# Kernel optimization log

Measured on AMD Instinct MI355X. Metric: run time of the kernel, lower is better.

The kernel has to match this reference:

```python
import jax, jax.numpy as jnp
import numpy as np

BS, N, H = 8, 2048, 512
NEG_INF = -1.0e9
LEAKY_SLOPE = 0.01  # torch nn.LeakyReLU default


def setup_inputs() -> dict:
    key = jax.random.key(0)
    ks = jax.random.split(key, 8)
    feats = jax.random.normal(ks[0], (BS, N, H), dtype=jnp.float32)
    # random 0/1 adjacency with self-loops so every row has >=1 neighbor
    adj = jax.random.randint(ks[1], (BS, N, N), 0, 2).astype(jnp.float32)
    adj = jnp.maximum(adj, jnp.eye(N, dtype=jnp.float32)[None])
    s = 1.0 / np.sqrt(H)
    return {
        "feats": feats,
        "adj_mat": adj,
        "fc_w": jax.random.normal(ks[2], (H, H), dtype=jnp.float32) * s,
        "fc_b": jax.random.normal(ks[3], (H,), dtype=jnp.float32) * s,
        "q_w": jax.random.normal(ks[4], (1, H), dtype=jnp.float32) * s,
        "q_b": jax.random.normal(ks[5], (1,), dtype=jnp.float32) * s,
        "k_w": jax.random.normal(ks[6], (1, H), dtype=jnp.float32) * s,
        "k_b": jax.random.normal(ks[7], (1,), dtype=jnp.float32) * s,
    }


def reference(feats, adj_mat, fc_w, fc_b, q_w, q_b, k_w, k_b):
    # feats: [bs, N, H]; torch Linear: x @ W.T + b
    feat_proj = jnp.einsum("bnh,oh->bno", feats, fc_w) + fc_b          # [bs, N, H]
    q = jnp.einsum("bnh,oh->bno", feat_proj, q_w) + q_b                # [bs, N, 1]
    k = jnp.einsum("bnh,oh->bno", feat_proj, k_w) + k_b                # [bs, N, 1]
    logits = q + jnp.swapaxes(k, 2, 1)                                 # [bs, N, N] broadcast add
    masked = logits + (1.0 - adj_mat) * NEG_INF
    masked = jnp.where(masked >= 0, masked, LEAKY_SLOPE * masked)      # LeakyReLU
    atten = jax.nn.softmax(masked, axis=-1)
    # dropout is identity in eval mode
    out = jnp.einsum("bnm,bmh->bnh", atten, feat_proj)
    return out + feats  # residual=True
```

## Files before the change

kernel.cpp:

```cpp
#include <hip/hip_runtime.h>
#include <hip/hip_bf16.h>
#include <cstdint>
#include <cstddef>

#define BSZ 8
#define NN 2048
#define HH 512
#define MROWS (BSZ * NN)
#define LOG2E 1.44269504088896f

typedef __attribute__((ext_vector_type(4))) float f32x4;
typedef __attribute__((ext_vector_type(8))) short short8;
typedef __attribute__((ext_vector_type(4))) unsigned short us4;
typedef __attribute__((ext_vector_type(4))) uint32_t u32x4;

#if __has_builtin(__builtin_amdgcn_exp2f)
#define EXP2(x) __builtin_amdgcn_exp2f(x)
#else
#define EXP2(x) __expf((x) * 0.69314718056f)
#endif

static __device__ __forceinline__ unsigned short f2bf(float f) {
    uint32_t u = __builtin_bit_cast(uint32_t, f);
    u += 0x7fffu + ((u >> 16) & 1u);
    return (unsigned short)(u >> 16);
}

static __device__ __forceinline__ void async16(const unsigned short* g, unsigned short* l) {
    __builtin_amdgcn_global_load_lds(
        (const __attribute__((address_space(1))) void*)g,
        (__attribute__((address_space(3))) void*)l, 16, 0, 0);
}

__global__ __launch_bounds__(256) void prep_kernel(
    const float* __restrict__ feats, const float* __restrict__ fc_w,
    unsigned short* __restrict__ feats_bf, unsigned short* __restrict__ fcw_bf) {
    const int bid = blockIdx.x;
    const int tid = threadIdx.x;
    if (bid < 2048) {
        const int base = bid * 1024 + tid;
#pragma unroll
        for (int j = 0; j < 4; ++j) {
            const int i = base + j * 256;
            f32x4 v = ((const f32x4*)feats)[i];
            us4 o;
#pragma unroll
            for (int c = 0; c < 4; ++c) o[c] = f2bf(v[c]);
            ((us4*)feats_bf)[i] = o;
        }
    } else {
        const int base = (bid - 2048) * 1024 + tid;
#pragma unroll
        for (int j = 0; j < 4; ++j) {
            const int i = base + j * 256;
            f32x4 v = ((const f32x4*)fc_w)[i];
            us4 o;
#pragma unroll
            for (int c = 0; c < 4; ++c) o[c] = f2bf(v[c]);
            ((us4*)fcw_bf)[i] = o;
        }
    }
}

__global__ __launch_bounds__(256) void k2_kernel(
    const unsigned short* __restrict__ A, const unsigned short* __restrict__ Bt,
    const float* __restrict__ fc_b, const float* __restrict__ q_w,
    const float* __restrict__ k_w, const float* __restrict__ adj,
    unsigned short* __restrict__ fpT, unsigned char* __restrict__ maskb,
    float* __restrict__ qpart, float* __restrict__ kpart) {
    __shared__ alignas(16) unsigned short As[3][64 * 32];
    __shared__ alignas(16) unsigned short Bs[3][128 * 32];
    __shared__ float qred[2][64], kred[2][64];
    const int bid = blockIdx.x;
    const int tid = threadIdx.x;
    const int wave = tid >> 6, lane = tid & 63;
    if (bid % 3 == 0) {
        const int g = bid / 3;
        const int wi = wave >> 1, wj = wave & 1;
        const int n0 = (g & 3) * 128;
        const int i0 = (g >> 2) * 64;
        const int K = HH;
        const int lrow = lane >> 2;
        const int lseg = (lane & 3) * 8;
        const int fro = (lane & 15) * 32 + (lane >> 4) * 8;
        f32x4 acc[2][4];
#pragma unroll
        for (int a = 0; a < 2; ++a)
#pragma unroll
            for (int c = 0; c < 4; ++c) acc[a][c] = (f32x4)(0.f);

        auto stage = [&](int buf, int k0) {
            const unsigned short* ga = A + (size_t)(i0 + wave * 16 + lrow) * K + k0 + lseg;
            async16(ga, &As[buf][(wave * 16) * 32]);
            const unsigned short* gb = Bt + (size_t)(n0 + wave * 32 + lrow) * K + k0 + lseg;
            async16(gb, &Bs[buf][(wave * 32) * 32]);
            async16(gb + (size_t)16 * K, &Bs[buf][(wave * 32 + 16) * 32]);
        };

        stage(0, 0);
        asm volatile("s_waitcnt vmcnt(0)" ::: "memory");
        __builtin_amdgcn_sched_barrier(0);
        __builtin_amdgcn_s_barrier();
        __builtin_amdgcn_sched_barrier(0);

        for (int j = 0; j < 16; ++j) {
            if (j < 15) {
                stage((j + 1) % 3, (j + 1) * 32);
                asm volatile("s_waitcnt vmcnt(3)" ::: "memory");
            } else {
                asm volatile("s_waitcnt vmcnt(0)" ::: "memory");
            }
            __builtin_amdgcn_sched_barrier(0);
            __builtin_amdgcn_s_barrier();
            __builtin_amdgcn_sched_barrier(0);
            const int p = j % 3;
            short8 af[2], bf[4];
#pragma unroll
            for (int t = 0; t < 2; ++t) af[t] = *(const short8*)&As[p][(wi * 32 + t * 16) * 32 + fro];
#pragma unroll
            for (int t = 0; t < 4; ++t) bf[t] = *(const short8*)&Bs[p][(wj * 64 + t * 16) * 32 + fro];
            __builtin_amdgcn_s_setprio(1);
#pragma unroll
            for (int it = 0; it < 2; ++it)
#pragma unroll
                for (int jt = 0; jt < 4; ++jt)
                    acc[it][jt] = __builtin_amdgcn_mfma_f32_16x16x32_bf16(af[it], bf[jt], acc[it][jt], 0, 0, 0);
            __builtin_amdgcn_s_setprio(0);
        }

        int colv[4]; float cbv[4], qwv[4], kwv[4];
#pragma unroll
        for (int jt = 0; jt < 4; ++jt) {
            colv[jt] = n0 + wj * 64 + jt * 16 + (lane & 15);
            cbv[jt] = fc_b[colv[jt]];
            qwv[jt] = q_w[colv[jt]];
            kwv[jt] = k_w[colv[jt]];
        }
        const int b = i0 >> 11;
        const int il = i0 & 2047;
#pragma unroll
        for (int jt = 0; jt < 4; ++jt) {
#pragma unroll
            for (int it = 0; it < 2; ++it) {
                const int rb = wi * 32 + it * 16 + ((lane >> 4) << 2);
                us4 o;
#pragma unroll
                for (int r = 0; r < 4; ++r) o[r] = f2bf(acc[it][jt][r] + cbv[jt]);
                *(us4*)(fpT + ((size_t)b * HH + colv[jt]) * NN + il + rb) = o;
            }
        }
#pragma unroll
        for (int it = 0; it < 2; ++it) {
#pragma unroll
            for (int r = 0; r < 4; ++r) {
                float pq = 0.f, pk = 0.f;
#pragma unroll
                for (int jt = 0; jt < 4; ++jt) {
                    float v = acc[it][jt][r] + cbv[jt];
                    pq += v * qwv[jt];
                    pk += v * kwv[jt];
                }
                for (int off = 1; off < 16; off <<= 1) {
                    pq += __shfl_xor(pq, off, 64);
                    pk += __shfl_xor(pk, off, 64);
                }
                if ((lane & 15) == 0) {
                    const int rr = wi * 32 + it * 16 + ((lane >> 4) << 2) + r;
                    qred[wj][rr] = pq;
                    kred[wj][rr] = pk;
                }
            }
        }
        __syncthreads();
        if (tid < 64) {
            const size_t o = (size_t)(n0 >> 7) * MROWS + i0 + tid;
            qpart[o] = qred[0][tid] + qred[1][tid];
            kpart[o] = kred[0][tid] + kred[1][tid];
        }
    } else {
        const int a = (bid / 3) * 2 + (bid % 3) - 1;
#pragma unroll
        for (int s = 0; s < 2; ++s) {
            const int row = a * 8 + s * 4 + wave;
            const float* ar2 = adj + (size_t)row * NN;
#pragma unroll
            for (int p = 0; p < 4; ++p) {
                f32x4 v0 = *(const f32x4*)&ar2[p * 512 + lane * 8];
                f32x4 v1 = *(const f32x4*)&ar2[p * 512 + lane * 8 + 4];
                float fb = v0[0] + 2.f * v0[1] + 4.f * v0[2] + 8.f * v0[3]
                         + 16.f * v1[0] + 32.f * v1[1] + 64.f * v1[2] + 128.f * v1[3];
                maskb[(size_t)row * 256 + p * 64 + lane] = (unsigned char)(unsigned int)fb;
            }
        }
    }
}

__global__ __launch_bounds__(256) void fused_pv_kernel(
    const unsigned short* __restrict__ fpT, const unsigned char* __restrict__ maskb,
    const float* __restrict__ qpart, const float* __restrict__ kpart,
    const float* __restrict__ q_b, const float* __restrict__ k_b,
    const float* __restrict__ feats, float* __restrict__ out) {
    __shared__ alignas(16) unsigned short As[3][64 * 32];
    __shared__ alignas(16) unsigned short Bs[3][256 * 32];
    __shared__ float kLDS[NN];
    __shared__ float qLDS[64];
    __shared__ float rzl[64];
    const int tid = threadIdx.x;
    const int wave = tid >> 6, lane = tid & 63;
    const int bid = blockIdx.x;
    const int b = bid & 7;
    const int t6 = bid >> 3;
    const int i0 = (t6 >> 1) * 64;
    const int n0 = (t6 & 1) * 256;
    const size_t rowbase = (size_t)b * NN + i0;

    {
        const float kb = k_b[0], qb = q_b[0];
#pragma unroll
        for (int s = 0; s < 8; ++s) {
            const int j = s * 256 + tid;
            const size_t gj = (size_t)b * NN + j;
            kLDS[j] = (kpart[gj] + kpart[MROWS + gj] + kpart[2 * MROWS + gj]
                     + kpart[3 * MROWS + gj] + kb) * LOG2E;
        }
        if (tid < 64) {
            const size_t gi = rowbase + tid;
            qLDS[tid] = (qpart[gi] + qpart[MROWS + gi] + qpart[2 * MROWS + gi]
                       + qpart[3 * MROWS + gi] + qb) * LOG2E;
        }
    }
    __syncthreads();

    const int r0 = tid >> 2;
    const int c8 = (tid & 3) * 8;
    const float qi = qLDS[r0];

    const unsigned short* Bt = fpT + (size_t)b * HH * NN;
    const uint32_t* mk = (const uint32_t*)maskb;
    const size_t mrow = (rowbase + r0) * 64;
    const int lrow = lane >> 2, lseg = (lane & 3) * 8;
    const int fro = (lane & 15) * 32 + (lane >> 4) * 8;

    auto stageB = [&](int buf, int k0) {
        const int rbase = wave * 64;
        const unsigned short* gb = Bt + (size_t)(n0 + rbase + lrow) * NN + k0 + lseg;
        async16(gb, &Bs[buf][rbase * 32]);
        async16(gb + (size_t)16 * NN, &Bs[buf][(rbase + 16) * 32]);
        async16(gb + (size_t)32 * NN, &Bs[buf][(rbase + 32) * 32]);
        async16(gb + (size_t)48 * NN, &Bs[buf][(rbase + 48) * 32]);
    };
    auto transform = [&](int buf, int k0, uint32_t mbits) {
        const f32x4 kv0 = *(const f32x4*)&kLDS[k0 + c8];
        const f32x4 kv1 = *(const f32x4*)&kLDS[k0 + c8 + 4];
        const uint32_t byte8 = (mbits >> c8) & 0xffu;
        float wv[8];
#pragma unroll
        for (int c = 0; c < 8; ++c) {
            float s = qi + (c < 4 ? kv0[c] : kv1[c - 4]);
            s = fmaxf(s, 0.01f * s);
            const float e = EXP2(s);
            wv[c] = ((byte8 >> c) & 1u) ? e : 0.f;
        }
        u32x4 pk;
#pragma unroll
        for (int p = 0; p < 4; ++p) {
            const uint32_t lo = __builtin_bit_cast(uint32_t, wv[2 * p]);
            const uint32_t hi = __builtin_bit_cast(uint32_t, wv[2 * p + 1]);
            pk[p] = __builtin_amdgcn_perm(hi, lo, 0x07060302u);
        }
        *(u32x4*)&As[buf][r0 * 32 + c8] = pk;
    };

    f32x4 acc[4][4];
#pragma unroll
    for (int a = 0; a < 4; ++a)
#pragma unroll
        for (int c = 0; c < 4; ++c) acc[a][c] = (f32x4)(0.f);
    f32x4 acc_z[4] = {(f32x4)(0.f), (f32x4)(0.f), (f32x4)(0.f), (f32x4)(0.f)};
    short8 ones;
#pragma unroll
    for (int j = 0; j < 8; ++j) ones[j] = (short)0x3F80;

    auto compute = [&](int rd) {
        short8 af[4], bf[4];
#pragma unroll
        for (int t = 0; t < 4; ++t) af[t] = *(const short8*)&As[rd][(t * 16) * 32 + fro];
#pragma unroll
        for (int t = 0; t < 4; ++t) bf[t] = *(const short8*)&Bs[rd][(wave * 64 + t * 16) * 32 + fro];
        __builtin_amdgcn_s_setprio(1);
#pragma unroll
        for (int it = 0; it < 4; ++it)
#pragma unroll
            for (int jt = 0; jt < 4; ++jt)
                acc[it][jt] = __builtin_amdgcn_mfma_f32_16x16x32_bf16(af[it], bf[jt], acc[it][jt], 0, 0, 0);
        if (wave == 0) {
#pragma unroll
            for (int it = 0; it < 4; ++it)
                acc_z[it] = __builtin_amdgcn_mfma_f32_16x16x32_bf16(af[it], ones, acc_z[it], 0, 0, 0);
        }
        __builtin_amdgcn_s_setprio(0);
    };

    uint32_t mw_cur = mk[mrow];
    uint32_t mw_nxt = mk[mrow + 1];
    stageB(0, 0);
    transform(0, 0, mw_cur);
    asm volatile("s_waitcnt vmcnt(0)" ::: "memory");
    __builtin_amdgcn_sched_barrier(0);
    asm volatile("s_waitcnt lgkmcnt(0)" ::: "memory");
    __builtin_amdgcn_s_barrier();
    __builtin_amdgcn_sched_barrier(0);

    for (int j = 0; j < 62; ++j) {
        const int k0 = j * 32;
        const int rd = j % 3, st = (j + 1) % 3;
        uint32_t mnn;
        {
            const uint32_t* ma = mk + mrow + j + 2;
            asm volatile("global_load_dword %0, %1, off"
                         : "=v"(mnn) : "v"(ma) : "memory");
        }
        stageB(st, k0 + 32);
        asm volatile("s_waitcnt vmcnt(5)" ::: "memory");
        __builtin_amdgcn_sched_barrier(0);
        transform(st, k0 + 32, mw_nxt);
        mw_nxt = mnn;
        asm volatile("s_waitcnt lgkmcnt(0)" ::: "memory");
        __builtin_amdgcn_sched_barrier(0);
        __builtin_amdgcn_s_barrier();
        __builtin_amdgcn_sched_barrier(0);
        compute(rd);
    }
    {
        const int k0 = 62 * 32;
        stageB(0, k0 + 32);
        asm volatile("s_waitcnt vmcnt(4)" ::: "memory");
        __builtin_amdgcn_sched_barrier(0);
        transform(0, k0 + 32, mw_nxt);
        asm volatile("s_waitcnt lgkmcnt(0)" ::: "memory");
        __builtin_amdgcn_sched_barrier(0);
        __builtin_amdgcn_s_barrier();
        __builtin_amdgcn_sched_barrier(0);
        compute(62 % 3);
    }
    {
        asm volatile("s_waitcnt vmcnt(0)" ::: "memory");
        __builtin_amdgcn_sched_barrier(0);
        asm volatile("s_waitcnt lgkmcnt(0)" ::: "memory");
        __builtin_amdgcn_s_barrier();
        __builtin_amdgcn_sched_barrier(0);
        compute(0);
    }

    if (wave == 0 && (lane & 15) == 0) {
#pragma unroll
        for (int it = 0; it < 4; ++it) {
            const int rb = it * 16 + ((lane >> 4) << 2);
#pragma unroll
            for (int r = 0; r < 4; ++r) rzl[rb + r] = 1.0f / acc_z[it][r];
        }
    }
    __syncthreads();

#pragma unroll
    for (int it = 0; it < 4; ++it) {
        const int rb = it * 16 + ((lane >> 4) << 2);
        float rv[4];
#pragma unroll
        for (int r = 0; r < 4; ++r) rv[r] = rzl[rb + r];
#pragma unroll
        for (int jt = 0; jt < 4; ++jt) {
            const int col = n0 + wave * 64 + jt * 16 + (lane & 15);
#pragma unroll
            for (int r = 0; r < 4; ++r) {
                const size_t idx = (rowbase + rb + r) * HH + col;
                out[idx] = acc[it][jt][r] * rv[r] + feats[idx];
            }
        }
    }
}

extern "C" void kernel_launch(void* const* d_in, const int* in_sizes, int n_in,
                              void* d_out, int out_size, void* d_ws, size_t ws_size,
                              hipStream_t stream) {
    const float* feats = (const float*)d_in[0];
    const float* adj   = (const float*)d_in[1];
    const float* fc_w  = (const float*)d_in[2];
    const float* fc_b  = (const float*)d_in[3];
    const float* q_w   = (const float*)d_in[4];
    const float* q_b   = (const float*)d_in[5];
    const float* k_w   = (const float*)d_in[6];
    const float* k_b   = (const float*)d_in[7];
    float* out = (float*)d_out;

    char* w = (char*)d_ws;
    auto alloc = [&](size_t bytes) {
        char* p = w;
        w += (bytes + 255) & ~(size_t)255;
        return p;
    };
    unsigned short* feats_bf = (unsigned short*)alloc((size_t)BSZ * NN * HH * 2);
    unsigned short* fcw_bf   = (unsigned short*)alloc((size_t)HH * HH * 2);
    unsigned short* fpT   = (unsigned short*)alloc((size_t)BSZ * HH * NN * 2);
    unsigned char*  maskb = (unsigned char*)alloc((size_t)MROWS * 256);
    float* qpart = (float*)alloc((size_t)4 * MROWS * 4);
    float* kpart = (float*)alloc((size_t)4 * MROWS * 4);

    prep_kernel<<<2112, 256, 0, stream>>>(feats, fc_w, feats_bf, fcw_bf);
    k2_kernel<<<3072, 256, 0, stream>>>(feats_bf, fcw_bf, fc_b, q_w, k_w, adj,
                                        fpT, maskb, qpart, kpart);
    fused_pv_kernel<<<512, 256, 0, stream>>>(
        fpT, maskb, qpart, kpart, q_b, k_b, feats, out);
}
```

Baseline: 306.0 us.

## Use 512 threads in fused PV kernel and simplify k2 GEMM pipeline to double buffering

The fused attention-PV kernel now runs 8 waves per block instead of 4. Each wave covers 32 output columns instead of 64, and each thread transforms 4 mask/weight entries instead of 8, which halves per-thread accumulator registers and the async loads issued per wave. The k2 projection GEMM drops its triple-buffered, manually waitcnt-tuned pipeline and the setprio hints in favour of plain double buffering with __syncthreads. That frees LDS but loses the explicit load/compute overlap. The extra waves aim to hide latency better, at the cost of more barrier participants and lower per-wave MFMA reuse of A fragments.

Measured after the change: 307.4 us. No clear change (+0.4%).

```diff
diff --git a/kernel.cpp b/kernel.cpp
--- a/kernel.cpp
+++ b/kernel.cpp
@@ -12,7 +12,7 @@
 typedef __attribute__((ext_vector_type(4))) float f32x4;
 typedef __attribute__((ext_vector_type(8))) short short8;
 typedef __attribute__((ext_vector_type(4))) unsigned short us4;
-typedef __attribute__((ext_vector_type(4))) uint32_t u32x4;
+typedef __attribute__((ext_vector_type(2))) uint32_t u32x2;
 
 #if __has_builtin(__builtin_amdgcn_exp2f)
 #define EXP2(x) __builtin_amdgcn_exp2f(x)
@@ -68,8 +68,8 @@
     const float* __restrict__ k_w, const float* __restrict__ adj,
     unsigned short* __restrict__ fpT, unsigned char* __restrict__ maskb,
     float* __restrict__ qpart, float* __restrict__ kpart) {
-    __shared__ alignas(16) unsigned short As[3][64 * 32];
-    __shared__ alignas(16) unsigned short Bs[3][128 * 32];
+    __shared__ alignas(16) unsigned short As[2][64 * 32];
+    __shared__ alignas(16) unsigned short Bs[2][128 * 32];
     __shared__ float qred[2][64], kred[2][64];
     const int bid = blockIdx.x;
     const int tid = threadIdx.x;
@@ -98,34 +98,22 @@
         };
 
         stage(0, 0);
-        asm volatile("s_waitcnt vmcnt(0)" ::: "memory");
-        __builtin_amdgcn_sched_barrier(0);
-        __builtin_amdgcn_s_barrier();
-        __builtin_amdgcn_sched_barrier(0);
-
-        for (int j = 0; j < 16; ++j) {
-            if (j < 15) {
-                stage((j + 1) % 3, (j + 1) * 32);
-                asm volatile("s_waitcnt vmcnt(3)" ::: "memory");
-            } else {
-                asm volatile("s_waitcnt vmcnt(0)" ::: "memory");
-            }
-            __builtin_amdgcn_sched_barrier(0);
-            __builtin_amdgcn_s_barrier();
-            __builtin_amdgcn_sched_barrier(0);
-            const int p = j % 3;
+        __syncthreads();
+
+        for (int k0 = 0; k0 < K; k0 += 32) {
+            const int p = (k0 >> 5) & 1;
+            if (k0 + 32 < K) stage(p ^ 1, k0 + 32);
             short8 af[2], bf[4];
 #pragma unroll
             for (int t = 0; t < 2; ++t) af[t] = *(const short8*)&As[p][(wi * 32 + t * 16) * 32 + fro];
 #pragma unroll
             for (int t = 0; t < 4; ++t) bf[t] = *(const short8*)&Bs[p][(wj * 64 + t * 16) * 32 + fro];
-            __builtin_amdgcn_s_setprio(1);
 #pragma unroll
             for (int it = 0; it < 2; ++it)
 #pragma unroll
                 for (int jt = 0; jt < 4; ++jt)
                     acc[it][jt] = __builtin_amdgcn_mfma_f32_16x16x32_bf16(af[it], bf[jt], acc[it][jt], 0, 0, 0);
-            __builtin_amdgcn_s_setprio(0);
+            __syncthreads();
         }
 
         int colv[4]; float cbv[4], qwv[4], kwv[4];
@@ -195,7 +183,7 @@
     }
 }
 
-__global__ __launch_bounds__(256) void fused_pv_kernel(
+__global__ __launch_bounds__(512) void fused_pv_kernel(
     const unsigned short* __restrict__ fpT, const unsigned char* __restrict__ maskb,
     const float* __restrict__ qpart, const float* __restrict__ kpart,
     const float* __restrict__ q_b, const float* __restrict__ k_b,
@@ -217,8 +205,8 @@
     {
         const float kb = k_b[0], qb = q_b[0];
 #pragma unroll
-        for (int s = 0; s < 8; ++s) {
-            const int j = s * 256 + tid;
+        for (int s = 0; s < 4; ++s) {
+            const int j = s * 512 + tid;
             const size_t gj = (size_t)b * NN + j;
             kLDS[j] = (kpart[gj] + kpart[MROWS + gj] + kpart[2 * MROWS + gj]
                      + kpart[3 * MROWS + gj] + kb) * LOG2E;
@@ -231,8 +219,8 @@
     }
     __syncthreads();
 
-    const int r0 = tid >> 2;
-    const int c8 = (tid & 3) * 8;
+    const int r0 = tid >> 3;
+    const int c4 = (tid & 7) * 4;
     const float qi = qLDS[r0];
 
     const unsigned short* Bt = fpT + (size_t)b * HH * NN;
@@ -242,56 +230,53 @@
     const int fro = (lane & 15) * 32 + (lane >> 4) * 8;
 
     auto stageB = [&](int buf, int k0) {
-        const int rbase = wave * 64;
+        const int rbase = wave * 32;
         const unsigned short* gb = Bt + (size_t)(n0 + rbase + lrow) * NN + k0 + lseg;
         async16(gb, &Bs[buf][rbase * 32]);
         async16(gb + (size_t)16 * NN, &Bs[buf][(rbase + 16) * 32]);
-        async16(gb + (size_t)32 * NN, &Bs[buf][(rbase + 32) * 32]);
-        async16(gb + (size_t)48 * NN, &Bs[buf][(rbase + 48) * 32]);
     };
     auto transform = [&](int buf, int k0, uint32_t mbits) {
-        const f32x4 kv0 = *(const f32x4*)&kLDS[k0 + c8];
-        const f32x4 kv1 = *(const f32x4*)&kLDS[k0 + c8 + 4];
-        const uint32_t byte8 = (mbits >> c8) & 0xffu;
-        float wv[8];
-#pragma unroll
-        for (int c = 0; c < 8; ++c) {
-            float s = qi + (c < 4 ? kv0[c] : kv1[c - 4]);
+        const f32x4 kv = *(const f32x4*)&kLDS[k0 + c4];
+        const uint32_t nib = (mbits >> c4) & 0xfu;
+        float wv[4];
+#pragma unroll
+        for (int c = 0; c < 4; ++c) {
+            float s = qi + kv[c];
             s = fmaxf(s, 0.01f * s);
             const float e = EXP2(s);
-            wv[c] = ((byte8 >> c) & 1u) ? e : 0.f;
-        }
-        u32x4 pk;
-#pragma unroll
-        for (int p = 0; p < 4; ++p) {
+            wv[c] = ((nib >> c) & 1u) ? e : 0.f;
+        }
+        u32x2 pk;
+#pragma unroll
+        for (int p = 0; p < 2; ++p) {
             const uint32_t lo = __builtin_bit_cast(uint32_t, wv[2 * p]);
             const uint32_t hi = __builtin_bit_cast(uint32_t, wv[2 * p + 1]);
             pk[p] = __builtin_amdgcn_perm(hi, lo, 0x07060302u);
         }
-        *(u32x4*)&As[buf][r0 * 32 + c8] = pk;
+        *(u32x2*)&As[buf][r0 * 32 + c4] = pk;
     };
 
-    f32x4 acc[4][4];
+    f32x4 acc[4][2];
 #pragma unroll
     for (int a = 0; a < 4; ++a)
 #pragma unroll
-        for (int c = 0; c < 4; ++c) acc[a][c] = (f32x4)(0.f);
+        for (int c = 0; c < 2; ++c) acc[a][c] = (f32x4)(0.f);
     f32x4 acc_z[4] = {(f32x4)(0.f), (f32x4)(0.f), (f32x4)(0.f), (f32x4)(0.f)};
     short8 ones;
 #pragma unroll
     for (int j = 0; j < 8; ++j) ones[j] = (short)0x3F80;
 
     auto compute = [&](int rd) {
-        short8 af[4], bf[4];
+        short8 af[4], bf[2];
 #pragma unroll
         for (int t = 0; t < 4; ++t) af[t] = *(const short8*)&As[rd][(t * 16) * 32 + fro];
 #pragma unroll
-        for (int t = 0; t < 4; ++t) bf[t] = *(const short8*)&Bs[rd][(wave * 64 + t * 16) * 32 + fro];
+        for (int t = 0; t < 2; ++t) bf[t] = *(const short8*)&Bs[rd][(wave * 32 + t * 16) * 32 + fro];
         __builtin_amdgcn_s_setprio(1);
 #pragma unroll
         for (int it = 0; it < 4; ++it)
 #pragma unroll
-            for (int jt = 0; jt < 4; ++jt)
+            for (int jt = 0; jt < 2; ++jt)
                 acc[it][jt] = __builtin_amdgcn_mfma_f32_16x16x32_bf16(af[it], bf[jt], acc[it][jt], 0, 0, 0);
         if (wave == 0) {
 #pragma unroll
@@ -321,7 +306,7 @@
                          : "=v"(mnn) : "v"(ma) : "memory");
         }
         stageB(st, k0 + 32);
-        asm volatile("s_waitcnt vmcnt(5)" ::: "memory");
+        asm volatile("s_waitcnt vmcnt(3)" ::: "memory");
         __builtin_amdgcn_sched_barrier(0);
         transform(st, k0 + 32, mw_nxt);
         mw_nxt = mnn;
@@ -334,7 +319,7 @@
     {
         const int k0 = 62 * 32;
         stageB(0, k0 + 32);
-        asm volatile("s_waitcnt vmcnt(4)" ::: "memory");
+        asm volatile("s_waitcnt vmcnt(2)" ::: "memory");
         __builtin_amdgcn_sched_barrier(0);
         transform(0, k0 + 32, mw_nxt);
         asm volatile("s_waitcnt lgkmcnt(0)" ::: "memory");
@@ -369,8 +354,8 @@
 #pragma unroll
         for (int r = 0; r < 4; ++r) rv[r] = rzl[rb + r];
 #pragma unroll
-        for (int jt = 0; jt < 4; ++jt) {
-            const int col = n0 + wave * 64 + jt * 16 + (lane & 15);
+        for (int jt = 0; jt < 2; ++jt) {
+            const int col = n0 + wave * 32 + jt * 16 + (lane & 15);
 #pragma unroll
             for (int r = 0; r < 4; ++r) {
                 const size_t idx = (rowbase + rb + r) * HH + col;
@@ -409,6 +394,6 @@
     prep_kernel<<<2112, 256, 0, stream>>>(feats, fc_w, feats_bf, fcw_bf);
     k2_kernel<<<3072, 256, 0, stream>>>(feats_bf, fcw_bf, fc_b, q_w, k_w, adj,
                                         fpT, maskb, qpart, kpart);
-    fused_pv_kernel<<<512, 256, 0, stream>>>(
+    fused_pv_kernel<<<512, 512, 0, stream>>>(
         fpT, maskb, qpart, kpart, q_b, k_b, feats, out);
 }
```
